# Optimization experiments

Hardware: AMD Instinct MI355X
Metric: run time of the kernel (lower is better)

## Reference

```python
import jax, jax.numpy as jnp
import numpy as np

B, T, C = 2, 2048, 1024
NH = 16
HD = C // NH  # 64
FF = 4 * C
EPS = 1e-5


def layer_norm(x, w, b):
    mu = jnp.mean(x, axis=-1, keepdims=True)
    var = jnp.mean(jnp.square(x - mu), axis=-1, keepdims=True)
    return (x - mu) * jax.lax.rsqrt(var + EPS) * w + b


def setup_inputs() -> dict:
    key = jax.random.key(0)
    ks = jax.random.split(key, 12)
    s_in = 1.0 / np.sqrt(C)
    s_ff = 1.0 / np.sqrt(FF)
    return {
        "x": jax.random.normal(ks[0], (B, T, C), jnp.float32),
        "ln1_w": jnp.ones((C,), jnp.float32),
        "ln1_b": jnp.zeros((C,), jnp.float32),
        "Wq": jax.random.normal(ks[1], (C, C), jnp.float32) * s_in,
        "Wk": jax.random.normal(ks[2], (C, C), jnp.float32) * s_in,
        "Wv": jax.random.normal(ks[3], (C, C), jnp.float32) * s_in,
        "Wp": jax.random.normal(ks[4], (C, C), jnp.float32) * s_in,
        "bp": jnp.zeros((C,), jnp.float32),
        "ln2_w": jnp.ones((C,), jnp.float32),
        "ln2_b": jnp.zeros((C,), jnp.float32),
        "W1": jax.random.normal(ks[5], (C, FF), jnp.float32) * s_in,
        "b1": jnp.zeros((FF,), jnp.float32),
        "W2": jax.random.normal(ks[6], (FF, C), jnp.float32) * s_ff,
        "b2": jnp.zeros((C,), jnp.float32),
    }


def reference(x, ln1_w, ln1_b, Wq, Wk, Wv, Wp, bp, ln2_w, ln2_b, W1, b1, W2, b2):
    scale = HD ** (-0.5)
    h = layer_norm(x, ln1_w, ln1_b)  # [B,T,C]
    # project and split heads: [B,T,NH,HD] -> [B,NH,T,HD]
    q = (h @ Wq).reshape(B, T, NH, HD).transpose(0, 2, 1, 3)
    k = (h @ Wk).reshape(B, T, NH, HD).transpose(0, 2, 1, 3)
    v = (h @ Wv).reshape(B, T, NH, HD).transpose(0, 2, 1, 3)
    scores = jnp.einsum("bhqd,bhkd->bhqk", q, k) * scale  # [B,NH,T,T]
    causal = jnp.tril(jnp.ones((T, T), jnp.bool_))
    scores = jnp.where(causal, scores, -jnp.inf)
    attn = jax.nn.softmax(scores, axis=-1)
    o = jnp.einsum("bhqk,bhkd->bhqd", attn, v)  # [B,NH,T,HD]
    o = o.transpose(0, 2, 1, 3).reshape(B, T, C)
    x = x + o @ Wp + bp
    h2 = layer_norm(x, ln2_w, ln2_b)
    x = x + jax.nn.relu(h2 @ W1 + b1) @ W2 + b2
    return x
```

## Files before the change

kernel.cpp:

```cpp
#include <hip/hip_runtime.h>
#include <hip/hip_bf16.h>

using u16 = unsigned short;
typedef short v8s __attribute__((ext_vector_type(8)));
typedef float v4f __attribute__((ext_vector_type(4)));

#define B_ 2
#define T_ 2048
#define C_ 1024
#define NH_ 16
#define HD_ 64
#define FF_ 4096
#define NT (B_*T_)
#define QKVC 3072

__device__ __forceinline__ u16 f2b(float f) {
  union { float f; unsigned int i; } v; v.f = f;
  unsigned int r = (v.i + 0x7FFFu + ((v.i >> 16) & 1u)) >> 16;
  return (u16)r;
}
__device__ __forceinline__ v4f mfma16(v8s a, v8s b, v4f c) {
  return __builtin_amdgcn_mfma_f32_16x16x32_bf16(a, b, c, 0, 0, 0);
}
__device__ __forceinline__ void glds16(const u16* g, u16* l) {
  __builtin_amdgcn_global_load_lds(
      (const __attribute__((address_space(1))) unsigned int*)g,
      (__attribute__((address_space(3))) unsigned int*)l, 16, 0, 0);
}

__global__ __launch_bounds__(256) void wcvt_kernel(const float* __restrict__ W,
    u16* __restrict__ Wt, int K, int N) {
  __shared__ float t[32][33];
  int tx = threadIdx.x & 31, ty = threadIdx.x >> 5;
  int n0 = blockIdx.x * 32, k0 = blockIdx.y * 32;
#pragma unroll
  for (int j = 0; j < 4; ++j)
    t[ty + j * 8][tx] = W[(size_t)(k0 + ty + j * 8) * N + n0 + tx];
  __syncthreads();
#pragma unroll
  for (int j = 0; j < 4; ++j)
    Wt[(size_t)(n0 + ty + j * 8) * K + k0 + tx] = f2b(t[tx][ty + j * 8]);
}

__global__ __launch_bounds__(256) void ln_kernel(const float* __restrict__ x,
    const float* __restrict__ w, const float* __restrict__ b, u16* __restrict__ y) {
  int row = blockIdx.x;
  int tid = threadIdx.x;
  const float* xr = x + (size_t)row * C_;
  float4 f4 = *(const float4*)&xr[tid * 4];
  float f[4] = {f4.x, f4.y, f4.z, f4.w};
  float s1 = 0.f, s2 = 0.f;
#pragma unroll
  for (int i = 0; i < 4; ++i) { s1 += f[i]; s2 += f[i] * f[i]; }
#pragma unroll
  for (int off = 32; off > 0; off >>= 1) {
    s1 += __shfl_down(s1, off);
    s2 += __shfl_down(s2, off);
  }
  __shared__ float red[10];
  int lane = tid & 63, wid = tid >> 6;
  if (lane == 0) { red[wid] = s1; red[4 + wid] = s2; }
  __syncthreads();
  if (tid == 0) {
    float a = red[0] + red[1] + red[2] + red[3];
    float q = red[4] + red[5] + red[6] + red[7];
    float mu = a * (1.f / C_);
    float var = q * (1.f / C_) - mu * mu;
    red[8] = mu; red[9] = rsqrtf(var + 1e-5f);
  }
  __syncthreads();
  float mu = red[8], rs = red[9];
  union { uint2 v; u16 s[4]; } st;
#pragma unroll
  for (int i = 0; i < 4; ++i) {
    int c = tid * 4 + i;
    st.s[i] = f2b((f[i] - mu) * rs * w[c] + b[c]);
  }
  *(uint2*)&y[(size_t)row * C_ + tid * 4] = st.v;
}

__global__ __launch_bounds__(256) void gemm_bt(const u16* __restrict__ X,
    const u16* __restrict__ Wt, const float* __restrict__ bias,
    const float* __restrict__ resf, u16* __restrict__ Yb, float* __restrict__ Yf,
    int M, int N, int K, int relu) {
  __shared__ __align__(16) u16 As[128 * 32];
  __shared__ __align__(16) u16 Bs[128 * 32];
  int tid = threadIdx.x, lane = tid & 63, w = tid >> 6;
  int wm = w >> 1, wn = w & 1, quad = lane >> 4, lcol = lane & 15;
  int m0 = blockIdx.y * 128, n0 = blockIdx.x * 128;
  v4f acc[4][4] = {};
  int sr = lane >> 2, sc = lane & 3;
  const u16* gA = X  + (size_t)(m0 + w * 32 + sr) * K + sc * 8;
  const u16* gB = Wt + (size_t)(n0 + w * 32 + sr) * K + sc * 8;
  u16* lA = As + (w * 32) * 32;
  u16* lB = Bs + (w * 32) * 32;
  for (int k0 = 0; k0 < K; k0 += 32) {
    __syncthreads();
    glds16(gA + k0, lA);
    glds16(gA + k0 + (size_t)16 * K, lA + 16 * 32);
    glds16(gB + k0, lB);
    glds16(gB + k0 + (size_t)16 * K, lB + 16 * 32);
    __syncthreads();
    v8s a[4], b[4];
#pragma unroll
    for (int i = 0; i < 4; ++i) {
      a[i] = *(v8s*)&As[(wm * 64 + i * 16 + lcol) * 32 + quad * 8];
      b[i] = *(v8s*)&Bs[(wn * 64 + i * 16 + lcol) * 32 + quad * 8];
    }
#pragma unroll
    for (int i = 0; i < 4; ++i)
#pragma unroll
      for (int j = 0; j < 4; ++j)
        acc[i][j] = mfma16(a[i], b[j], acc[i][j]);
  }
#pragma unroll
  for (int i = 0; i < 4; ++i) {
    int mb = m0 + wm * 64 + i * 16 + quad * 4;
#pragma unroll
    for (int j = 0; j < 4; ++j) {
      int n = n0 + wn * 64 + j * 16 + lcol;
#pragma unroll
      for (int r = 0; r < 4; ++r) {
        float v = acc[i][j][r];
        if (bias) v += bias[n];
        if (resf) v += resf[(size_t)(mb + r) * N + n];
        if (relu) v = fmaxf(v, 0.f);
        if (Yb) Yb[(size_t)(mb + r) * N + n] = f2b(v);
        else    Yf[(size_t)(mb + r) * N + n] = v;
      }
    }
  }
}

__global__ __launch_bounds__(256) void gemm_bt_n64(const u16* __restrict__ X,
    const u16* __restrict__ Wt, const float* __restrict__ bias,
    const float* __restrict__ resf, u16* __restrict__ Yb, float* __restrict__ Yf,
    int M, int N, int K, int relu) {
  __shared__ __align__(16) u16 As[128 * 32];
  __shared__ __align__(16) u16 Bs[64 * 32];
  int tid = threadIdx.x, lane = tid & 63, w = tid >> 6;
  int wm = w >> 1, wn = w & 1, quad = lane >> 4, lcol = lane & 15;
  int m0 = blockIdx.y * 128, n0 = blockIdx.x * 64;
  v4f acc[4][2] = {};
  int sr = lane >> 2, sc = lane & 3;
  const u16* gA = X  + (size_t)(m0 + w * 32 + sr) * K + sc * 8;
  const u16* gB = Wt + (size_t)(n0 + w * 16 + sr) * K + sc * 8;
  u16* lA = As + (w * 32) * 32;
  u16* lB = Bs + (w * 16) * 32;
  for (int k0 = 0; k0 < K; k0 += 32) {
    __syncthreads();
    glds16(gA + k0, lA);
    glds16(gA + k0 + (size_t)16 * K, lA + 16 * 32);
    glds16(gB + k0, lB);
    __syncthreads();
    v8s a[4], b[2];
#pragma unroll
    for (int i = 0; i < 4; ++i)
      a[i] = *(v8s*)&As[(wm * 64 + i * 16 + lcol) * 32 + quad * 8];
#pragma unroll
    for (int j = 0; j < 2; ++j)
      b[j] = *(v8s*)&Bs[(wn * 32 + j * 16 + lcol) * 32 + quad * 8];
#pragma unroll
    for (int i = 0; i < 4; ++i)
#pragma unroll
      for (int j = 0; j < 2; ++j)
        acc[i][j] = mfma16(a[i], b[j], acc[i][j]);
  }
#pragma unroll
  for (int i = 0; i < 4; ++i) {
    int mb = m0 + wm * 64 + i * 16 + quad * 4;
#pragma unroll
    for (int j = 0; j < 2; ++j) {
      int n = n0 + wn * 32 + j * 16 + lcol;
#pragma unroll
      for (int r = 0; r < 4; ++r) {
        float v = acc[i][j][r];
        if (bias) v += bias[n];
        if (resf) v += resf[(size_t)(mb + r) * N + n];
        if (relu) v = fmaxf(v, 0.f);
        if (Yb) Yb[(size_t)(mb + r) * N + n] = f2b(v);
        else    Yf[(size_t)(mb + r) * N + n] = v;
      }
    }
  }
}

__global__ __launch_bounds__(256) void vt_kernel(const u16* __restrict__ QKV,
    u16* __restrict__ VT) {
  int bh = blockIdx.x, tt = blockIdx.y;
  int b = bh >> 4, h = bh & 15;
  int tid = threadIdx.x;
  __shared__ u16 L[64 * 72];
  int r = tid >> 2, g = tid & 3;
  size_t row = ((size_t)(b * T_ + tt * 64 + r)) * QKVC + 2 * C_ + h * HD_;
  union { uint4 v; u16 s[8]; } a0, a1;
  a0.v = *(const uint4*)&QKV[row + g * 8];
  a1.v = *(const uint4*)&QKV[row + 32 + g * 8];
#pragma unroll
  for (int e = 0; e < 8; ++e) L[(g * 8 + e) * 72 + r] = a0.s[e];
#pragma unroll
  for (int e = 0; e < 8; ++e) L[(32 + g * 8 + e) * 72 + r] = a1.s[e];
  __syncthreads();
  size_t orow = ((size_t)(bh * 64 + r)) * T_ + tt * 64;
  *(uint4*)&VT[orow + g * 8]      = *(uint4*)&L[r * 72 + g * 8];
  *(uint4*)&VT[orow + 32 + g * 8] = *(uint4*)&L[r * 72 + 32 + g * 8];
}

__global__ __launch_bounds__(256) void attn_kernel(const u16* __restrict__ QKV,
    const u16* __restrict__ VT, u16* __restrict__ Ob) {
  int bh = blockIdx.x, qt = blockIdx.y;
  int b = bh >> 4, h = bh & 15;
  int tid = threadIdx.x, lane = tid & 63, wid = tid >> 6;
  int quad = lane >> 4, lcol = lane & 15;
  __shared__ __align__(16) u16 Qs[64 * 72];
  __shared__ __align__(16) u16 Ks[64 * 72];
  __shared__ __align__(16) u16 Vs[64 * 72];
  __shared__ __align__(16) u16 Ps[4][16 * 72];
  int r = tid >> 2, g = tid & 3;
  size_t qrow = ((size_t)(b * T_ + qt * 64 + r)) * QKVC + h * HD_;
  *(uint4*)&Qs[r * 72 + g * 8]      = *(const uint4*)&QKV[qrow + g * 8];
  *(uint4*)&Qs[r * 72 + 32 + g * 8] = *(const uint4*)&QKV[qrow + 32 + g * 8];
  __syncthreads();
  v8s bq0 = *(v8s*)&Qs[(wid * 16 + lcol) * 72 + quad * 8];
  v8s bq1 = *(v8s*)&Qs[(wid * 16 + lcol) * 72 + 32 + quad * 8];
  float m_i = -__builtin_inff(), l_i = 0.f;
  v4f accO[4] = {};
  int q_glob = qt * 64 + wid * 16 + lcol;
  const float SC = 0.125f * 1.44269504f;
  for (int kb = 0; kb <= qt; ++kb) {
    __syncthreads();
    size_t krow = ((size_t)(b * T_ + kb * 64 + r)) * QKVC + C_ + h * HD_;
    *(uint4*)&Ks[r * 72 + g * 8]      = *(const uint4*)&QKV[krow + g * 8];
    *(uint4*)&Ks[r * 72 + 32 + g * 8] = *(const uint4*)&QKV[krow + 32 + g * 8];
    size_t vrow = ((size_t)(bh * 64 + r)) * T_ + kb * 64;
    *(uint4*)&Vs[r * 72 + g * 8]      = *(const uint4*)&VT[vrow + g * 8];
    *(uint4*)&Vs[r * 72 + 32 + g * 8] = *(const uint4*)&VT[vrow + 32 + g * 8];
    __syncthreads();
    v4f s[4];
#pragma unroll
    for (int cg = 0; cg < 4; ++cg) {
      v4f acc = {};
      v8s ak0 = *(v8s*)&Ks[(cg * 16 + lcol) * 72 + quad * 8];
      v8s ak1 = *(v8s*)&Ks[(cg * 16 + lcol) * 72 + 32 + quad * 8];
      acc = mfma16(ak0, bq0, acc);
      acc = mfma16(ak1, bq1, acc);
      s[cg] = acc;
    }
    float mx = -__builtin_inff();
#pragma unroll
    for (int cg = 0; cg < 4; ++cg)
#pragma unroll
      for (int rg = 0; rg < 4; ++rg) {
        int kt = kb * 64 + cg * 16 + quad * 4 + rg;
        float v = (kt <= q_glob) ? s[cg][rg] : -__builtin_inff();
        s[cg][rg] = v;
        mx = fmaxf(mx, v);
      }
    mx = fmaxf(mx, __shfl_xor(mx, 16));
    mx = fmaxf(mx, __shfl_xor(mx, 32));
    float mnew = fmaxf(m_i, mx);
    float alpha = exp2f((m_i - mnew) * SC);
    float base = mnew * SC;
    float ps = 0.f;
#pragma unroll
    for (int cg = 0; cg < 4; ++cg) {
      union { u16 s4[4]; unsigned long long ll; } pk;
#pragma unroll
      for (int rg = 0; rg < 4; ++rg) {
        float pv = exp2f(s[cg][rg] * SC - base);
        ps += pv;
        pk.s4[rg] = f2b(pv);
      }
      *(unsigned long long*)&Ps[wid][lcol * 72 + cg * 16 + quad * 4] = pk.ll;
    }
    ps += __shfl_xor(ps, 16);
    ps += __shfl_xor(ps, 32);
    l_i = l_i * alpha + ps;
    m_i = mnew;
#pragma unroll
    for (int df = 0; df < 4; ++df)
#pragma unroll
      for (int rg = 0; rg < 4; ++rg) accO[df][rg] *= alpha;
    v8s bp0 = *(v8s*)&Ps[wid][lcol * 72 + quad * 8];
    v8s bp1 = *(v8s*)&Ps[wid][lcol * 72 + 32 + quad * 8];
#pragma unroll
    for (int df = 0; df < 4; ++df) {
      v8s av0 = *(v8s*)&Vs[(df * 16 + lcol) * 72 + quad * 8];
      v8s av1 = *(v8s*)&Vs[(df * 16 + lcol) * 72 + 32 + quad * 8];
      accO[df] = mfma16(av0, bp0, accO[df]);
      accO[df] = mfma16(av1, bp1, accO[df]);
    }
  }
  float inv = 1.f / l_i;
  size_t orow = ((size_t)(b * T_ + qt * 64 + wid * 16 + lcol)) * C_ + h * HD_;
#pragma unroll
  for (int df = 0; df < 4; ++df) {
    union { u16 s4[4]; unsigned long long ll; } ok;
#pragma unroll
    for (int rg = 0; rg < 4; ++rg) ok.s4[rg] = f2b(accO[df][rg] * inv);
    *(unsigned long long*)&Ob[orow + df * 16 + quad * 4] = ok.ll;
  }
}

extern "C" void kernel_launch(void* const* d_in, const int* in_sizes, int n_in,
                              void* d_out, int out_size, void* d_ws, size_t ws_size,
                              hipStream_t stream) {
  (void)in_sizes; (void)n_in; (void)out_size; (void)ws_size;
  const float* x    = (const float*)d_in[0];
  const float* ln1w = (const float*)d_in[1];
  const float* ln1b = (const float*)d_in[2];
  const float* Wq   = (const float*)d_in[3];
  const float* Wk   = (const float*)d_in[4];
  const float* Wv   = (const float*)d_in[5];
  const float* Wp   = (const float*)d_in[6];
  const float* bp   = (const float*)d_in[7];
  const float* ln2w = (const float*)d_in[8];
  const float* ln2b = (const float*)d_in[9];
  const float* W1   = (const float*)d_in[10];
  const float* b1   = (const float*)d_in[11];
  const float* W2   = (const float*)d_in[12];
  const float* b2   = (const float*)d_in[13];
  float* out = (float*)d_out;
  char* ws = (char*)d_ws;
  const size_t MB = 1024 * 1024;
  u16*   h1    = (u16*)(ws);
  u16*   VT    = (u16*)(ws);
  u16*   QKVb  = (u16*)(ws + 8  * MB);
  u16*   Ob    = (u16*)(ws + 32 * MB);
  float* xa    = (float*)(ws + 40 * MB);
  u16*   h2    = (u16*)(ws);
  u16*   f1    = (u16*)(ws + 8 * MB);
  u16*   Wqkvt = (u16*)(ws + 56 * MB);
  u16*   Wpt   = (u16*)(ws + 62 * MB);
  u16*   W1t   = (u16*)(ws + 64 * MB);
  u16*   W2t   = (u16*)(ws + 72 * MB);

  wcvt_kernel<<<dim3(32, 32),  256, 0, stream>>>(Wq, Wqkvt,                1024, 1024);
  wcvt_kernel<<<dim3(32, 32),  256, 0, stream>>>(Wk, Wqkvt + 1024 * 1024,  1024, 1024);
  wcvt_kernel<<<dim3(32, 32),  256, 0, stream>>>(Wv, Wqkvt + 2048 * 1024,  1024, 1024);
  wcvt_kernel<<<dim3(32, 32),  256, 0, stream>>>(Wp, Wpt,                  1024, 1024);
  wcvt_kernel<<<dim3(128, 32), 256, 0, stream>>>(W1, W1t,                  1024, 4096);
  wcvt_kernel<<<dim3(32, 128), 256, 0, stream>>>(W2, W2t,                  4096, 1024);

  ln_kernel<<<NT, 256, 0, stream>>>(x, ln1w, ln1b, h1);
  gemm_bt<<<dim3(QKVC / 128, NT / 128), 256, 0, stream>>>(h1, Wqkvt, nullptr, nullptr, QKVb, nullptr, NT, QKVC, C_, 0);
  vt_kernel<<<dim3(B_ * NH_, T_ / 64), 256, 0, stream>>>(QKVb, VT);
  attn_kernel<<<dim3(B_ * NH_, T_ / 64), 256, 0, stream>>>(QKVb, VT, Ob);
  gemm_bt_n64<<<dim3(C_ / 64, NT / 128), 256, 0, stream>>>(Ob, Wpt, bp, x, nullptr, xa, NT, C_, C_, 0);
  ln_kernel<<<NT, 256, 0, stream>>>(xa, ln2w, ln2b, h2);
  gemm_bt<<<dim3(FF_ / 128, NT / 128), 256, 0, stream>>>(h2, W1t, b1, nullptr, f1, nullptr, NT, FF_, C_, 1);
  gemm_bt_n64<<<dim3(C_ / 64, NT / 128), 256, 0, stream>>>(f1, W2t, b2, xa, nullptr, out, NT, C_, FF_, 0);
}
```

Before: 461.6 us.

## Enlarge attention query tile to 128 and split-K the FFN down-projection

The attention kernel now handles 128 queries per block, with each warp owning two 16-row query subtiles. Each K/V tile loaded into shared memory is reused for twice as many queries, halving the number of blocks and the K/V reload traffic. The cost is extra masked work on the diagonal blocks and larger per-block register and LDS use. The final W2 GEMM switches to the 128x128 kernel with a two-way K split; the partial sums go to a workspace buffer and a new elementwise kernel adds them together with the bias and residual, which costs an extra pass over the output.

```diff
diff --git a/kernel.cpp b/kernel.cpp
--- a/kernel.cpp
+++ b/kernel.cpp
@@ -82,24 +82,25 @@
 __global__ __launch_bounds__(256) void gemm_bt(const u16* __restrict__ X,
     const u16* __restrict__ Wt, const float* __restrict__ bias,
     const float* __restrict__ resf, u16* __restrict__ Yb, float* __restrict__ Yf,
-    int M, int N, int K, int relu) {
+    float* __restrict__ Yfz1, int M, int N, int lda, int ldb, int kspl, int relu) {
   __shared__ __align__(16) u16 As[128 * 32];
   __shared__ __align__(16) u16 Bs[128 * 32];
   int tid = threadIdx.x, lane = tid & 63, w = tid >> 6;
   int wm = w >> 1, wn = w & 1, quad = lane >> 4, lcol = lane & 15;
   int m0 = blockIdx.y * 128, n0 = blockIdx.x * 128;
+  int koff = blockIdx.z * kspl;
   v4f acc[4][4] = {};
   int sr = lane >> 2, sc = lane & 3;
-  const u16* gA = X  + (size_t)(m0 + w * 32 + sr) * K + sc * 8;
-  const u16* gB = Wt + (size_t)(n0 + w * 32 + sr) * K + sc * 8;
+  const u16* gA = X  + (size_t)(m0 + w * 32 + sr) * lda + koff + sc * 8;
+  const u16* gB = Wt + (size_t)(n0 + w * 32 + sr) * ldb + koff + sc * 8;
   u16* lA = As + (w * 32) * 32;
   u16* lB = Bs + (w * 32) * 32;
-  for (int k0 = 0; k0 < K; k0 += 32) {
+  for (int k0 = 0; k0 < kspl; k0 += 32) {
     __syncthreads();
     glds16(gA + k0, lA);
-    glds16(gA + k0 + (size_t)16 * K, lA + 16 * 32);
+    glds16(gA + k0 + (size_t)16 * lda, lA + 16 * 32);
     glds16(gB + k0, lB);
-    glds16(gB + k0 + (size_t)16 * K, lB + 16 * 32);
+    glds16(gB + k0 + (size_t)16 * ldb, lB + 16 * 32);
     __syncthreads();
     v8s a[4], b[4];
 #pragma unroll
@@ -113,6 +114,7 @@
       for (int j = 0; j < 4; ++j)
         acc[i][j] = mfma16(a[i], b[j], acc[i][j]);
   }
+  float* yf = blockIdx.z ? Yfz1 : Yf;
 #pragma unroll
   for (int i = 0; i < 4; ++i) {
     int mb = m0 + wm * 64 + i * 16 + quad * 4;
@@ -126,7 +128,7 @@
         if (resf) v += resf[(size_t)(mb + r) * N + n];
         if (relu) v = fmaxf(v, 0.f);
         if (Yb) Yb[(size_t)(mb + r) * N + n] = f2b(v);
-        else    Yf[(size_t)(mb + r) * N + n] = v;
+        else    yf[(size_t)(mb + r) * N + n] = v;
       }
     }
   }
@@ -185,6 +187,22 @@
   }
 }
 
+__global__ __launch_bounds__(256) void add4_kernel(float* __restrict__ out,
+    const float* __restrict__ p0, const float* __restrict__ bias,
+    const float* __restrict__ res) {
+  size_t e0 = ((size_t)blockIdx.x * 256 + threadIdx.x) * 4;
+  int col = (int)(e0 & (C_ - 1));
+  float4 o = *(float4*)&out[e0];
+  float4 p = *(const float4*)&p0[e0];
+  float4 r = *(const float4*)&res[e0];
+  float4 bb = *(const float4*)&bias[col];
+  o.x += p.x + r.x + bb.x;
+  o.y += p.y + r.y + bb.y;
+  o.z += p.z + r.z + bb.z;
+  o.w += p.w + r.w + bb.w;
+  *(float4*)&out[e0] = o;
+}
+
 __global__ __launch_bounds__(256) void vt_kernel(const u16* __restrict__ QKV,
     u16* __restrict__ VT) {
   int bh = blockIdx.x, tt = blockIdx.y;
@@ -212,93 +230,118 @@
   int b = bh >> 4, h = bh & 15;
   int tid = threadIdx.x, lane = tid & 63, wid = tid >> 6;
   int quad = lane >> 4, lcol = lane & 15;
-  __shared__ __align__(16) u16 Qs[64 * 72];
+  __shared__ __align__(16) u16 Qs[128 * 72];
   __shared__ __align__(16) u16 Ks[64 * 72];
   __shared__ __align__(16) u16 Vs[64 * 72];
-  __shared__ __align__(16) u16 Ps[4][16 * 72];
-  int r = tid >> 2, g = tid & 3;
-  size_t qrow = ((size_t)(b * T_ + qt * 64 + r)) * QKVC + h * HD_;
-  *(uint4*)&Qs[r * 72 + g * 8]      = *(const uint4*)&QKV[qrow + g * 8];
-  *(uint4*)&Qs[r * 72 + 32 + g * 8] = *(const uint4*)&QKV[qrow + 32 + g * 8];
+  __shared__ __align__(16) u16 Ps[4][32 * 72];
+  {
+    int r = tid >> 1, g = tid & 1;
+    size_t qrow = ((size_t)(b * T_ + qt * 128 + r)) * QKVC + h * HD_ + g * 32;
+#pragma unroll
+    for (int c = 0; c < 4; ++c)
+      *(uint4*)&Qs[r * 72 + g * 32 + c * 8] = *(const uint4*)&QKV[qrow + c * 8];
+  }
   __syncthreads();
-  v8s bq0 = *(v8s*)&Qs[(wid * 16 + lcol) * 72 + quad * 8];
-  v8s bq1 = *(v8s*)&Qs[(wid * 16 + lcol) * 72 + 32 + quad * 8];
-  float m_i = -__builtin_inff(), l_i = 0.f;
-  v4f accO[4] = {};
-  int q_glob = qt * 64 + wid * 16 + lcol;
+  v8s bq[2][2];
+#pragma unroll
+  for (int j = 0; j < 2; ++j)
+#pragma unroll
+    for (int kh = 0; kh < 2; ++kh)
+      bq[j][kh] = *(v8s*)&Qs[(wid * 32 + j * 16 + lcol) * 72 + kh * 32 + quad * 8];
+  float m_i[2] = {-__builtin_inff(), -__builtin_inff()};
+  float l_i[2] = {0.f, 0.f};
+  v4f accO[4][2] = {};
+  int qg[2];
+#pragma unroll
+  for (int j = 0; j < 2; ++j) qg[j] = qt * 128 + wid * 32 + j * 16 + lcol;
   const float SC = 0.125f * 1.44269504f;
-  for (int kb = 0; kb <= qt; ++kb) {
-    __syncthreads();
-    size_t krow = ((size_t)(b * T_ + kb * 64 + r)) * QKVC + C_ + h * HD_;
-    *(uint4*)&Ks[r * 72 + g * 8]      = *(const uint4*)&QKV[krow + g * 8];
-    *(uint4*)&Ks[r * 72 + 32 + g * 8] = *(const uint4*)&QKV[krow + 32 + g * 8];
-    size_t vrow = ((size_t)(bh * 64 + r)) * T_ + kb * 64;
-    *(uint4*)&Vs[r * 72 + g * 8]      = *(const uint4*)&VT[vrow + g * 8];
-    *(uint4*)&Vs[r * 72 + 32 + g * 8] = *(const uint4*)&VT[vrow + 32 + g * 8];
-    __syncthreads();
-    v4f s[4];
-#pragma unroll
-    for (int cg = 0; cg < 4; ++cg) {
-      v4f acc = {};
-      v8s ak0 = *(v8s*)&Ks[(cg * 16 + lcol) * 72 + quad * 8];
-      v8s ak1 = *(v8s*)&Ks[(cg * 16 + lcol) * 72 + 32 + quad * 8];
-      acc = mfma16(ak0, bq0, acc);
-      acc = mfma16(ak1, bq1, acc);
-      s[cg] = acc;
-    }
-    float mx = -__builtin_inff();
+  int kr = tid >> 2, kg = tid & 3;
+  int nkb = 2 * qt + 2;
+  for (int kb = 0; kb < nkb; ++kb) {
+    __syncthreads();
+    size_t krow = ((size_t)(b * T_ + kb * 64 + kr)) * QKVC + C_ + h * HD_;
+    *(uint4*)&Ks[kr * 72 + kg * 8]      = *(const uint4*)&QKV[krow + kg * 8];
+    *(uint4*)&Ks[kr * 72 + 32 + kg * 8] = *(const uint4*)&QKV[krow + 32 + kg * 8];
+    size_t vrow = ((size_t)(bh * 64 + kr)) * T_ + kb * 64;
+    *(uint4*)&Vs[kr * 72 + kg * 8]      = *(const uint4*)&VT[vrow + kg * 8];
+    *(uint4*)&Vs[kr * 72 + 32 + kg * 8] = *(const uint4*)&VT[vrow + 32 + kg * 8];
+    __syncthreads();
+    v8s ak[4][2];
 #pragma unroll
     for (int cg = 0; cg < 4; ++cg)
 #pragma unroll
-      for (int rg = 0; rg < 4; ++rg) {
-        int kt = kb * 64 + cg * 16 + quad * 4 + rg;
-        float v = (kt <= q_glob) ? s[cg][rg] : -__builtin_inff();
-        s[cg][rg] = v;
-        mx = fmaxf(mx, v);
+      for (int kh = 0; kh < 2; ++kh)
+        ak[cg][kh] = *(v8s*)&Ks[(cg * 16 + lcol) * 72 + kh * 32 + quad * 8];
+#pragma unroll
+    for (int j = 0; j < 2; ++j) {
+      v4f s[4];
+#pragma unroll
+      for (int cg = 0; cg < 4; ++cg) {
+        v4f acc = {};
+        acc = mfma16(ak[cg][0], bq[j][0], acc);
+        acc = mfma16(ak[cg][1], bq[j][1], acc);
+        s[cg] = acc;
       }
-    mx = fmaxf(mx, __shfl_xor(mx, 16));
-    mx = fmaxf(mx, __shfl_xor(mx, 32));
-    float mnew = fmaxf(m_i, mx);
-    float alpha = exp2f((m_i - mnew) * SC);
-    float base = mnew * SC;
-    float ps = 0.f;
-#pragma unroll
-    for (int cg = 0; cg < 4; ++cg) {
-      union { u16 s4[4]; unsigned long long ll; } pk;
-#pragma unroll
-      for (int rg = 0; rg < 4; ++rg) {
-        float pv = exp2f(s[cg][rg] * SC - base);
-        ps += pv;
-        pk.s4[rg] = f2b(pv);
+      float mx = -__builtin_inff();
+#pragma unroll
+      for (int cg = 0; cg < 4; ++cg)
+#pragma unroll
+        for (int rg = 0; rg < 4; ++rg) {
+          int kt = kb * 64 + cg * 16 + quad * 4 + rg;
+          float v = (kt <= qg[j]) ? s[cg][rg] : -__builtin_inff();
+          s[cg][rg] = v;
+          mx = fmaxf(mx, v);
+        }
+      mx = fmaxf(mx, __shfl_xor(mx, 16));
+      mx = fmaxf(mx, __shfl_xor(mx, 32));
+      float mnew = fmaxf(m_i[j], mx);
+      float alpha = exp2f((m_i[j] - mnew) * SC);
+      float base = mnew * SC;
+      float ps = 0.f;
+#pragma unroll
+      for (int cg = 0; cg < 4; ++cg) {
+        union { u16 s4[4]; unsigned long long ll; } pk;
+#pragma unroll
+        for (int rg = 0; rg < 4; ++rg) {
+          float pv = exp2f(s[cg][rg] * SC - base);
+          ps += pv;
+          pk.s4[rg] = f2b(pv);
+        }
+        *(unsigned long long*)&Ps[wid][(j * 16 + lcol) * 72 + cg * 16 + quad * 4] = pk.ll;
       }
-      *(unsigned long long*)&Ps[wid][lcol * 72 + cg * 16 + quad * 4] = pk.ll;
-    }
-    ps += __shfl_xor(ps, 16);
-    ps += __shfl_xor(ps, 32);
-    l_i = l_i * alpha + ps;
-    m_i = mnew;
-#pragma unroll
-    for (int df = 0; df < 4; ++df)
-#pragma unroll
-      for (int rg = 0; rg < 4; ++rg) accO[df][rg] *= alpha;
-    v8s bp0 = *(v8s*)&Ps[wid][lcol * 72 + quad * 8];
-    v8s bp1 = *(v8s*)&Ps[wid][lcol * 72 + 32 + quad * 8];
+      ps += __shfl_xor(ps, 16);
+      ps += __shfl_xor(ps, 32);
+      l_i[j] = l_i[j] * alpha + ps;
+      m_i[j] = mnew;
+#pragma unroll
+      for (int df = 0; df < 4; ++df)
+#pragma unroll
+        for (int rg = 0; rg < 4; ++rg) accO[df][j][rg] *= alpha;
+    }
+#pragma unroll
+    for (int j = 0; j < 2; ++j) {
+      v8s bp0 = *(v8s*)&Ps[wid][(j * 16 + lcol) * 72 + quad * 8];
+      v8s bp1 = *(v8s*)&Ps[wid][(j * 16 + lcol) * 72 + 32 + quad * 8];
+#pragma unroll
+      for (int df = 0; df < 4; ++df) {
+        v8s av0 = *(v8s*)&Vs[(df * 16 + lcol) * 72 + quad * 8];
+        v8s av1 = *(v8s*)&Vs[(df * 16 + lcol) * 72 + 32 + quad * 8];
+        accO[df][j] = mfma16(av0, bp0, accO[df][j]);
+        accO[df][j] = mfma16(av1, bp1, accO[df][j]);
+      }
+    }
+  }
+#pragma unroll
+  for (int j = 0; j < 2; ++j) {
+    float inv = 1.f / l_i[j];
+    size_t orow = ((size_t)(b * T_ + qg[j])) * C_ + h * HD_;
 #pragma unroll
     for (int df = 0; df < 4; ++df) {
-      v8s av0 = *(v8s*)&Vs[(df * 16 + lcol) * 72 + quad * 8];
-      v8s av1 = *(v8s*)&Vs[(df * 16 + lcol) * 72 + 32 + quad * 8];
-      accO[df] = mfma16(av0, bp0, accO[df]);
-      accO[df] = mfma16(av1, bp1, accO[df]);
-    }
-  }
-  float inv = 1.f / l_i;
-  size_t orow = ((size_t)(b * T_ + qt * 64 + wid * 16 + lcol)) * C_ + h * HD_;
-#pragma unroll
-  for (int df = 0; df < 4; ++df) {
-    union { u16 s4[4]; unsigned long long ll; } ok;
-#pragma unroll
-    for (int rg = 0; rg < 4; ++rg) ok.s4[rg] = f2b(accO[df][rg] * inv);
-    *(unsigned long long*)&Ob[orow + df * 16 + quad * 4] = ok.ll;
+      union { u16 s4[4]; unsigned long long ll; } ok;
+#pragma unroll
+      for (int rg = 0; rg < 4; ++rg) ok.s4[rg] = f2b(accO[df][j][rg] * inv);
+      *(unsigned long long*)&Ob[orow + df * 16 + quad * 4] = ok.ll;
+    }
   }
 }
 
@@ -334,6 +377,7 @@
   u16*   Wpt   = (u16*)(ws + 62 * MB);
   u16*   W1t   = (u16*)(ws + 64 * MB);
   u16*   W2t   = (u16*)(ws + 72 * MB);
+  float* p0    = (float*)(ws + 56 * MB);
 
   wcvt_kernel<<<dim3(32, 32),  256, 0, stream>>>(Wq, Wqkvt,                1024, 1024);
   wcvt_kernel<<<dim3(32, 32),  256, 0, stream>>>(Wk, Wqkvt + 1024 * 1024,  1024, 1024);
@@ -343,11 +387,16 @@
   wcvt_kernel<<<dim3(32, 128), 256, 0, stream>>>(W2, W2t,                  4096, 1024);
 
   ln_kernel<<<NT, 256, 0, stream>>>(x, ln1w, ln1b, h1);
-  gemm_bt<<<dim3(QKVC / 128, NT / 128), 256, 0, stream>>>(h1, Wqkvt, nullptr, nullptr, QKVb, nullptr, NT, QKVC, C_, 0);
+  gemm_bt<<<dim3(QKVC / 128, NT / 128, 1), 256, 0, stream>>>(
+      h1, Wqkvt, nullptr, nullptr, QKVb, nullptr, nullptr, NT, QKVC, C_, C_, C_, 0);
   vt_kernel<<<dim3(B_ * NH_, T_ / 64), 256, 0, stream>>>(QKVb, VT);
-  attn_kernel<<<dim3(B_ * NH_, T_ / 64), 256, 0, stream>>>(QKVb, VT, Ob);
-  gemm_bt_n64<<<dim3(C_ / 64, NT / 128), 256, 0, stream>>>(Ob, Wpt, bp, x, nullptr, xa, NT, C_, C_, 0);
+  attn_kernel<<<dim3(B_ * NH_, T_ / 128), 256, 0, stream>>>(QKVb, VT, Ob);
+  gemm_bt_n64<<<dim3(C_ / 64, NT / 128), 256, 0, stream>>>(
+      Ob, Wpt, bp, x, nullptr, xa, NT, C_, C_, 0);
   ln_kernel<<<NT, 256, 0, stream>>>(xa, ln2w, ln2b, h2);
-  gemm_bt<<<dim3(FF_ / 128, NT / 128), 256, 0, stream>>>(h2, W1t, b1, nullptr, f1, nullptr, NT, FF_, C_, 1);
-  gemm_bt_n64<<<dim3(C_ / 64, NT / 128), 256, 0, stream>>>(f1, W2t, b2, xa, nullptr, out, NT, C_, FF_, 0);
-}
+  gemm_bt<<<dim3(FF_ / 128, NT / 128, 1), 256, 0, stream>>>(
+      h2, W1t, b1, nullptr, f1, nullptr, nullptr, NT, FF_, C_, C_, C_, 1);
+  gemm_bt<<<dim3(C_ / 128, NT / 128, 2), 256, 0, stream>>>(
+      f1, W2t, nullptr, nullptr, nullptr, p0, out, NT, C_, FF_, FF_, FF_ / 2, 0);
+  add4_kernel<<<(NT * C_) / (256 * 4), 256, 0, stream>>>(out, p0, b2, xa);
+}
```

Result: no change. 463.2 us (+0.3%).
